# Performance work log

Measured on AMD Instinct MI355X. Metric: run time of the kernel, lower is better.

The kernel has to match this reference:

```python
import jax, jax.numpy as jnp
import numpy as np

N = 50000      # nodes
E = 800000     # edges
F_IN = 128     # input node feature dim
H = 4          # attention heads
DH = 64        # per-head hidden dim
HID = H * DH   # 256
NEG_SLOPE = 0.2


def gat_conv(h, src, dst, W, al, ar, b, res):
    # DGL GATConv: project, compute attention logits, edge softmax over dst, aggregate.
    feat = (h @ W).reshape(N, H, DH)                      # [N,H,DH]
    el = jnp.einsum('nhd,hd->nh', feat, al)               # [N,H]
    er = jnp.einsum('nhd,hd->nh', feat, ar)               # [N,H]
    e = el[src] + er[dst]                                 # [E,H]
    e = jnp.where(e > 0, e, NEG_SLOPE * e)                # LeakyReLU(0.2)
    m = jax.ops.segment_max(e, dst, num_segments=N)       # [N,H]
    m = jnp.where(jnp.isfinite(m), m, 0.0)                # zero-in-degree safety
    ex = jnp.exp(e - m[dst])                              # [E,H]
    denom = jax.ops.segment_sum(ex, dst, num_segments=N)  # [N,H]
    alpha = ex / jnp.maximum(denom[dst], 1e-16)           # edge softmax
    out = jax.ops.segment_sum(feat[src] * alpha[:, :, None], dst, num_segments=N)
    return out + res.reshape(N, H, DH) + b.reshape(1, H, DH)


def setup_inputs() -> dict:
    key = jax.random.key(0)
    ks = jax.random.split(key, 16)
    x = jax.random.normal(ks[0], (N, F_IN), jnp.float32)
    edge_index = jax.random.randint(ks[1], (2, E), 0, N)
    s_in = 1.0 / np.sqrt(F_IN)
    s_h = 1.0 / np.sqrt(HID)
    W0 = jax.random.normal(ks[2], (F_IN, HID), jnp.float32) * s_in
    W1 = jax.random.normal(ks[3], (HID, HID), jnp.float32) * s_h
    W2 = jax.random.normal(ks[4], (HID, HID), jnp.float32) * s_h
    al0 = jax.random.normal(ks[5], (H, DH), jnp.float32) * 0.1
    al1 = jax.random.normal(ks[6], (H, DH), jnp.float32) * 0.1
    al2 = jax.random.normal(ks[7], (H, DH), jnp.float32) * 0.1
    ar0 = jax.random.normal(ks[8], (H, DH), jnp.float32) * 0.1
    ar1 = jax.random.normal(ks[9], (H, DH), jnp.float32) * 0.1
    ar2 = jax.random.normal(ks[10], (H, DH), jnp.float32) * 0.1
    b0 = jnp.zeros((HID,), jnp.float32)
    b1 = jnp.zeros((HID,), jnp.float32)
    b2 = jnp.zeros((HID,), jnp.float32)
    resW0 = jax.random.normal(ks[11], (F_IN, HID), jnp.float32) * s_in
    return {"x": x, "edge_index": edge_index,
            "W0": W0, "W1": W1, "W2": W2,
            "al0": al0, "al1": al1, "al2": al2,
            "ar0": ar0, "ar1": ar1, "ar2": ar2,
            "b0": b0, "b1": b1, "b2": b2,
            "resW0": resW0}


def reference(x, edge_index, W0, W1, W2, al0, al1, al2, ar0, ar1, ar2, b0, b1, b2, resW0):
    src, dst = edge_index[0], edge_index[1]
    # layer 0: residual via linear projection (in != heads*hidden)
    h = gat_conv(x, src, dst, W0, al0, ar0, b0, x @ resW0).reshape(N, HID)
    h = jax.nn.relu(h)
    # layer 1: identity residual
    h = gat_conv(h, src, dst, W1, al1, ar1, b1, h).reshape(N, HID)
    h = jax.nn.relu(h)
    # layer 2: identity residual, mean over heads
    h = gat_conv(h, src, dst, W2, al2, ar2, b2, h)
    return h.mean(axis=1)  # [N, DH]
```

## Files before the change

### kernel.cpp

```cpp
#include <hip/hip_runtime.h>
#include <math.h>

#define N_NODES 50000
#define N_EDGES 800000
#define F_INPUT 128
#define HEADS 4
#define DHID 64
#define HID 256
#define M_PAD 50048
#define SCAN_B 49

typedef _Float16 half8 __attribute__((ext_vector_type(8)));
typedef _Float16 half4 __attribute__((ext_vector_type(4)));
typedef float f32x4 __attribute__((ext_vector_type(4)));


__global__ void hist_kernel(const int* __restrict__ dst, int* __restrict__ counts) {
    int e = blockIdx.x * 256 + threadIdx.x;
    if (e < N_EDGES) atomicAdd(&counts[dst[e]], 1);
}

__global__ __launch_bounds__(256) void scan1_kernel(const int* __restrict__ counts,
                                                    int* __restrict__ pre,
                                                    int* __restrict__ bsum) {
    __shared__ int buf[256];
    int tid = threadIdx.x;
    int idx = blockIdx.x * 1024 + tid * 4;
    int v0 = 0, v1 = 0, v2 = 0, v3 = 0;
    if (idx + 3 < N_NODES) {
        int4 v = *(const int4*)&counts[idx];
        v0 = v.x; v1 = v.y; v2 = v.z; v3 = v.w;
    } else {
        if (idx + 0 < N_NODES) v0 = counts[idx + 0];
        if (idx + 1 < N_NODES) v1 = counts[idx + 1];
        if (idx + 2 < N_NODES) v2 = counts[idx + 2];
        if (idx + 3 < N_NODES) v3 = counts[idx + 3];
    }
    int s0 = v0, s1 = s0 + v1, s2 = s1 + v2, s3 = s2 + v3;
    buf[tid] = s3;
    __syncthreads();
    for (int off = 1; off < 256; off <<= 1) {
        int t = (tid >= off) ? buf[tid - off] : 0;
        __syncthreads();
        buf[tid] += t;
        __syncthreads();
    }
    int excl = buf[tid] - s3;
    if (idx + 0 < N_NODES) pre[idx + 0] = excl + s0;
    if (idx + 1 < N_NODES) pre[idx + 1] = excl + s1;
    if (idx + 2 < N_NODES) pre[idx + 2] = excl + s2;
    if (idx + 3 < N_NODES) pre[idx + 3] = excl + s3;
    if (tid == 255) bsum[blockIdx.x] = buf[255];
}

__global__ void scan2_kernel(const int* __restrict__ bsum, int* __restrict__ bpre) {
    int lane = threadIdx.x;
    int v = (lane < SCAN_B) ? bsum[lane] : 0;
    int orig = v;
#pragma unroll
    for (int off = 1; off < 64; off <<= 1) {
        int t = __shfl_up(v, off, 64);
        if (lane >= off) v += t;
    }
    if (lane < SCAN_B) bpre[lane] = v - orig;
}

__global__ __launch_bounds__(256) void scan3_kernel(const int* __restrict__ pre,
                                                    const int* __restrict__ bpre,
                                                    int* __restrict__ row_ptr) {
    int add = bpre[blockIdx.x];
    int idx = blockIdx.x * 1024 + threadIdx.x * 4;
#pragma unroll
    for (int u = 0; u < 4; u++) {
        int i = idx + u;
        if (i < N_NODES) row_ptr[i + 1] = pre[i] + add;
    }
    if (blockIdx.x == 0 && threadIdx.x == 0) row_ptr[0] = 0;
}

__global__ void scatter_kernel(const int* __restrict__ src, const int* __restrict__ dst,
                               const int* __restrict__ row_ptr, int* __restrict__ cursor,
                               int* __restrict__ esrc) {
    int e = blockIdx.x * 256 + threadIdx.x;
    if (e < N_EDGES) {
        int d = dst[e];
        int pos = row_ptr[d] + atomicAdd(&cursor[d], 1);
        esrc[pos] = src[e];
    }
}


__global__ void cvt_x_kernel(const float* __restrict__ x, _Float16* __restrict__ x16) {
    int t = blockIdx.x * 256 + threadIdx.x;
    if (t < N_NODES * F_INPUT / 4) {
        f32x4 v = *(const f32x4*)&x[t * 4];
        half4 h = {(_Float16)v.x, (_Float16)v.y, (_Float16)v.z, (_Float16)v.w};
        *(half4*)&x16[(size_t)t * 4] = h;
    }
}

__global__ void wt_all_kernel(const float* __restrict__ W0, _Float16* __restrict__ Wt0,
                              const float* __restrict__ WR, _Float16* __restrict__ WtR,
                              const float* __restrict__ W1, _Float16* __restrict__ Wt1,
                              const float* __restrict__ W2, _Float16* __restrict__ Wt2) {
    int t = blockIdx.x * 256 + threadIdx.x;
    const float* W; _Float16* Wt; int K; int u;
    if (t < 32768)        { W = W0; Wt = Wt0; K = F_INPUT; u = t; }
    else if (t < 65536)   { W = WR; Wt = WtR; K = F_INPUT; u = t - 32768; }
    else if (t < 131072)  { W = W1; Wt = Wt1; K = HID;     u = t - 65536; }
    else if (t < 196608)  { W = W2; Wt = Wt2; K = HID;     u = t - 131072; }
    else return;
    int k = u >> 8;
    int c = u & 255;
    Wt[(size_t)c * K + k] = (_Float16)W[u];
}


__device__ __forceinline__ void gl2lds16(const void* g, void* l) {
    __builtin_amdgcn_global_load_lds((const __attribute__((address_space(1))) void*)g,
                                     (__attribute__((address_space(3))) void*)l, 16, 0, 0);
}

__global__ __launch_bounds__(256) void mfma_gemm(const _Float16* __restrict__ A16,
                                                 const _Float16* __restrict__ Wt,
                                                 _Float16* __restrict__ out16,
                                                 float* __restrict__ out32,
                                                 int K) {
    __shared__ __align__(16) _Float16 As[4 * 512];
    __shared__ __align__(16) _Float16 Ws[16 * 512];
    int tid = threadIdx.x;
    int w = tid >> 6;
    int lane = tid & 63;
    int lrow = lane & 15;
    int lk = lane >> 4;
    int row0 = blockIdx.x * 64;

    f32x4 acc[4][4] = {};
    const _Float16* Abase = A16 + (size_t)(row0 + w * 16 + lrow) * K + lk * 8;

    for (int k0 = 0; k0 < K; k0 += 32) {
        gl2lds16(Abase + k0, &As[w * 512]);
#pragma unroll
        for (int i = 0; i < 4; i++) {
            int tt = i * 4 + w;
            gl2lds16(Wt + (size_t)(tt * 16 + lrow) * K + k0 + lk * 8, &Ws[tt * 512]);
        }
        __syncthreads();
        half8 a[4], b[4];
#pragma unroll
        for (int m = 0; m < 4; m++) a[m] = *(const half8*)&As[m * 512 + lane * 8];
#pragma unroll
        for (int j = 0; j < 4; j++) b[j] = *(const half8*)&Ws[(w * 4 + j) * 512 + lane * 8];
#pragma unroll
        for (int m = 0; m < 4; m++)
#pragma unroll
            for (int j = 0; j < 4; j++)
                acc[m][j] = __builtin_amdgcn_mfma_f32_16x16x32_f16(a[m], b[j], acc[m][j], 0, 0, 0);
        __syncthreads();
    }

#pragma unroll
    for (int m = 0; m < 4; m++) {
#pragma unroll
        for (int r = 0; r < 4; r++) {
            int grow = row0 + m * 16 + lk * 4 + r;
            if (grow < N_NODES) {
                if (out16) {
#pragma unroll
                    for (int j = 0; j < 4; j++)
                        out16[(size_t)grow * HID + w * 64 + j * 16 + lrow] = (_Float16)acc[m][j][r];
                } else {
#pragma unroll
                    for (int j = 0; j < 4; j++)
                        out32[(size_t)grow * HID + w * 64 + j * 16 + lrow] = acc[m][j][r];
                }
            }
        }
    }
}


__global__ __launch_bounds__(256) void elr_kernel(const _Float16* __restrict__ feat16,
                                                  const float* __restrict__ al,
                                                  const float* __restrict__ ar,
                                                  float* __restrict__ el, float* __restrict__ er) {
    int n = blockIdx.x * 4 + (threadIdx.x >> 6);
    int lane = threadIdx.x & 63;
    half4 f = *(const half4*)&feat16[(size_t)n * HID + lane * 4];
    f32x4 a = *(const f32x4*)&al[lane * 4];
    f32x4 r = *(const f32x4*)&ar[lane * 4];
    float pl = (float)f.x * a.x + (float)f.y * a.y + (float)f.z * a.z + (float)f.w * a.w;
    float pr = (float)f.x * r.x + (float)f.y * r.y + (float)f.z * r.z + (float)f.w * r.w;
#pragma unroll
    for (int off = 1; off < 16; off <<= 1) {
        pl += __shfl_xor(pl, off, 64);
        pr += __shfl_xor(pr, off, 64);
    }
    if ((lane & 15) == 0) {
        int h = lane >> 4;
        el[n * HEADS + h] = pl;
        er[n * HEADS + h] = pr;
    }
}


__global__ __launch_bounds__(256) void agg_kernel(const _Float16* __restrict__ feat16,
                                                  const float* __restrict__ el,
                                                  const float* __restrict__ er,
                                                  const int* __restrict__ row_ptr,
                                                  const int* __restrict__ esrc,
                                                  const float* __restrict__ res,
                                                  const float* __restrict__ bias,
                                                  float* __restrict__ out32,
                                                  _Float16* __restrict__ out16,
                                                  float* __restrict__ outmean,
                                                  int do_relu) {
    __shared__ float lds[4][64 * 5];
    int wv = threadIdx.x >> 6;
    int lane = threadIdx.x & 63;
    int n = blockIdx.x * 4 + wv;
    int head = lane >> 4;
    int start = row_ptr[n];
    int deg = row_ptr[n + 1] - start;
    f32x4 ern = *(const f32x4*)&er[n * 4];
    float* L = lds[wv];

    f32x4 mx = {-1e30f, -1e30f, -1e30f, -1e30f};
    f32x4 acc = {0.f, 0.f, 0.f, 0.f};
    float smh = 0.f;

    for (int base = 0; base < deg; base += 64) {
        int e = base + lane;
        int s = 0;
        f32x4 x = {-1e30f, -1e30f, -1e30f, -1e30f};
        if (e < deg) {
            s = esrc[start + e];
            f32x4 v = *(const f32x4*)&el[s * 4];
            v = v + ern;
            x.x = v.x > 0.f ? v.x : 0.2f * v.x;
            x.y = v.y > 0.f ? v.y : 0.2f * v.y;
            x.z = v.z > 0.f ? v.z : 0.2f * v.z;
            x.w = v.w > 0.f ? v.w : 0.2f * v.w;
        }
        f32x4 cm = x;
#pragma unroll
        for (int off = 1; off < 64; off <<= 1) {
            cm.x = fmaxf(cm.x, __shfl_xor(cm.x, off, 64));
            cm.y = fmaxf(cm.y, __shfl_xor(cm.y, off, 64));
            cm.z = fmaxf(cm.z, __shfl_xor(cm.z, off, 64));
            cm.w = fmaxf(cm.w, __shfl_xor(cm.w, off, 64));
        }
        f32x4 nmx;
        nmx.x = fmaxf(mx.x, cm.x);
        nmx.y = fmaxf(mx.y, cm.y);
        nmx.z = fmaxf(mx.z, cm.z);
        nmx.w = fmaxf(mx.w, cm.w);
        float mxh  = (head == 0) ? mx.x  : (head == 1) ? mx.y  : (head == 2) ? mx.z  : mx.w;
        float nmxh = (head == 0) ? nmx.x : (head == 1) ? nmx.y : (head == 2) ? nmx.z : nmx.w;
        float sc = __expf(mxh - nmxh);
        smh *= sc;
        acc = acc * sc;
        f32x4 ex4;
        ex4.x = __expf(x.x - nmx.x);
        ex4.y = __expf(x.y - nmx.y);
        ex4.z = __expf(x.z - nmx.z);
        ex4.w = __expf(x.w - nmx.w);
        L[lane * 5 + 0] = ex4.x;
        L[lane * 5 + 1] = ex4.y;
        L[lane * 5 + 2] = ex4.z;
        L[lane * 5 + 3] = ex4.w;
        L[lane * 5 + 4] = __int_as_float(s);
        f32x4 cs = ex4;
#pragma unroll
        for (int off = 1; off < 64; off <<= 1) {
            cs.x += __shfl_xor(cs.x, off, 64);
            cs.y += __shfl_xor(cs.y, off, 64);
            cs.z += __shfl_xor(cs.z, off, 64);
            cs.w += __shfl_xor(cs.w, off, 64);
        }
        smh += (head == 0) ? cs.x : (head == 1) ? cs.y : (head == 2) ? cs.z : cs.w;

        int cnt = min(64, deg - base);
        int j = 0;
        for (; j + 4 <= cnt; j += 4) {
            float exv[4]; int ssv[4];
#pragma unroll
            for (int u = 0; u < 4; u++) {
                exv[u] = L[(j + u) * 5 + head];
                ssv[u] = __float_as_int(L[(j + u) * 5 + 4]);
            }
            half4 f[4];
#pragma unroll
            for (int u = 0; u < 4; u++)
                f[u] = *(const half4*)&feat16[(size_t)ssv[u] * HID + lane * 4];
#pragma unroll
            for (int u = 0; u < 4; u++) {
                acc.x += exv[u] * (float)f[u].x;
                acc.y += exv[u] * (float)f[u].y;
                acc.z += exv[u] * (float)f[u].z;
                acc.w += exv[u] * (float)f[u].w;
            }
        }
        for (; j < cnt; j++) {
            float ex = L[j * 5 + head];
            int ss = __float_as_int(L[j * 5 + 4]);
            half4 f = *(const half4*)&feat16[(size_t)ss * HID + lane * 4];
            acc.x += ex * (float)f.x;
            acc.y += ex * (float)f.y;
            acc.z += ex * (float)f.z;
            acc.w += ex * (float)f.w;
        }
        mx = nmx;
    }

    float inv = 1.f / fmaxf(smh, 1e-16f);
    f32x4 o = acc * inv;
    o = o + *(const f32x4*)&res[(size_t)n * HID + lane * 4] + *(const f32x4*)&bias[lane * 4];
    if (do_relu) {
        o.x = fmaxf(o.x, 0.f);
        o.y = fmaxf(o.y, 0.f);
        o.z = fmaxf(o.z, 0.f);
        o.w = fmaxf(o.w, 0.f);
    }
    if (outmean) {
        o.x += __shfl_xor(o.x, 16, 64); o.x += __shfl_xor(o.x, 32, 64);
        o.y += __shfl_xor(o.y, 16, 64); o.y += __shfl_xor(o.y, 32, 64);
        o.z += __shfl_xor(o.z, 16, 64); o.z += __shfl_xor(o.z, 32, 64);
        o.w += __shfl_xor(o.w, 16, 64); o.w += __shfl_xor(o.w, 32, 64);
        if (head == 0) {
            f32x4 mo = o * 0.25f;
            *(f32x4*)&outmean[(size_t)n * DHID + (lane & 15) * 4] = mo;
        }
    } else {
        *(f32x4*)&out32[(size_t)n * HID + lane * 4] = o;
        half4 h = {(_Float16)o.x, (_Float16)o.y, (_Float16)o.z, (_Float16)o.w};
        *(half4*)&out16[(size_t)n * HID + lane * 4] = h;
    }
}


extern "C" void kernel_launch(void* const* d_in, const int* in_sizes, int n_in,
                              void* d_out, int out_size, void* d_ws, size_t ws_size,
                              hipStream_t stream) {
    const float* x     = (const float*)d_in[0];
    const int*   ei    = (const int*)d_in[1];
    const float* W0    = (const float*)d_in[2];
    const float* W1    = (const float*)d_in[3];
    const float* W2    = (const float*)d_in[4];
    const float* al0   = (const float*)d_in[5];
    const float* al1   = (const float*)d_in[6];
    const float* al2   = (const float*)d_in[7];
    const float* ar0   = (const float*)d_in[8];
    const float* ar1   = (const float*)d_in[9];
    const float* ar2   = (const float*)d_in[10];
    const float* b0    = (const float*)d_in[11];
    const float* b1    = (const float*)d_in[12];
    const float* b2    = (const float*)d_in[13];
    const float* resW0 = (const float*)d_in[14];
    float* out = (float*)d_out;

    const int* srcp = ei;
    const int* dstp = ei + N_EDGES;

    char* p = (char*)d_ws;
    auto alloc = [&](size_t bytes) -> char* {
        char* r = p;
        p += (bytes + 255) & ~(size_t)255;
        return r;
    };
    float*     H32    = (float*)alloc((size_t)N_NODES * HID * 4);
    _Float16*  H16    = (_Float16*)alloc((size_t)M_PAD * HID * 2);
    _Float16*  feat16 = (_Float16*)alloc((size_t)M_PAD * HID * 2);
    _Float16*  x16    = (_Float16*)alloc((size_t)M_PAD * F_INPUT * 2);
    float*     el     = (float*)alloc((size_t)N_NODES * HEADS * 4);
    float*     er     = (float*)alloc((size_t)N_NODES * HEADS * 4);
    _Float16*  Wt0    = (_Float16*)alloc((size_t)HID * F_INPUT * 2);
    _Float16*  WtR    = (_Float16*)alloc((size_t)HID * F_INPUT * 2);
    _Float16*  Wt1    = (_Float16*)alloc((size_t)HID * HID * 2);
    _Float16*  Wt2    = (_Float16*)alloc((size_t)HID * HID * 2);
    int*       counts = (int*)alloc((size_t)N_NODES * 4);
    int*       rowptr = (int*)alloc((size_t)(N_NODES + 1) * 4);
    int*       esrc   = (int*)alloc((size_t)N_EDGES * 4);
    int*       pre    = (int*)alloc((size_t)N_NODES * 4);
    int*       bsum   = (int*)alloc((size_t)SCAN_B * 4);
    int*       bpre   = (int*)alloc((size_t)SCAN_B * 4);

    const int EB = (N_EDGES + 255) / 256;
    const int GB = M_PAD / 64;
    const int NB = N_NODES / 4;

    hipMemsetAsync(counts, 0, (size_t)N_NODES * 4, stream);
    hist_kernel<<<EB, 256, 0, stream>>>(dstp, counts);
    scan1_kernel<<<SCAN_B, 256, 0, stream>>>(counts, pre, bsum);
    scan2_kernel<<<1, 64, 0, stream>>>(bsum, bpre);
    scan3_kernel<<<SCAN_B, 256, 0, stream>>>(pre, bpre, rowptr);
    hipMemsetAsync(counts, 0, (size_t)N_NODES * 4, stream);
    scatter_kernel<<<EB, 256, 0, stream>>>(srcp, dstp, rowptr, counts, esrc);

    cvt_x_kernel<<<(N_NODES * F_INPUT / 4 + 255) / 256, 256, 0, stream>>>(x, x16);
    wt_all_kernel<<<768, 256, 0, stream>>>(W0, Wt0, resW0, WtR, W1, Wt1, W2, Wt2);

    mfma_gemm<<<GB, 256, 0, stream>>>(x16, WtR, nullptr, H32, F_INPUT);
    mfma_gemm<<<GB, 256, 0, stream>>>(x16, Wt0, feat16, nullptr, F_INPUT);
    elr_kernel<<<NB, 256, 0, stream>>>(feat16, al0, ar0, el, er);
    agg_kernel<<<NB, 256, 0, stream>>>(feat16, el, er, rowptr, esrc, H32, b0, H32, H16, nullptr, 1);

    mfma_gemm<<<GB, 256, 0, stream>>>(H16, Wt1, feat16, nullptr, HID);
    elr_kernel<<<NB, 256, 0, stream>>>(feat16, al1, ar1, el, er);
    agg_kernel<<<NB, 256, 0, stream>>>(feat16, el, er, rowptr, esrc, H32, b1, H32, H16, nullptr, 1);

    mfma_gemm<<<GB, 256, 0, stream>>>(H16, Wt2, feat16, nullptr, HID);
    elr_kernel<<<NB, 256, 0, stream>>>(feat16, al2, ar2, el, er);
    agg_kernel<<<NB, 256, 0, stream>>>(feat16, el, er, rowptr, esrc, H32, b2, nullptr, nullptr, out, 0);
}
```

Baseline: 549.2 us.

## Fuse attention logits into GEMM epilogues and merge layer-0 projections

The per-head el/er dot products move into the MFMA GEMM epilogue, computed from the fp32 accumulators with lane shuffles, so the three separate elr kernels and their re-reads of feat16 go away. Layer 0 packs W0 and resW0 into one 512-column transposed weight and computes feature and residual projections in a single 512-thread kernel, loading the input tile once. The hidden-layer GEMM uses 128-row tiles with 8 waves to share the weight tile more widely. The aggregation kernel gets a single-pass softmax path for nodes with degree at most 64, and the two counter memsets become one; the extra epilogue work and larger blocks may raise register pressure.

```diff
diff --git a/kernel.cpp b/kernel.cpp
--- a/kernel.cpp
+++ b/kernel.cpp
@@ -34,7 +34,6 @@
         if (idx + 0 < N_NODES) v0 = counts[idx + 0];
         if (idx + 1 < N_NODES) v1 = counts[idx + 1];
         if (idx + 2 < N_NODES) v2 = counts[idx + 2];
-        if (idx + 3 < N_NODES) v3 = counts[idx + 3];
     }
     int s0 = v0, s1 = s0 + v1, s2 = s1 + v2, s3 = s2 + v3;
     buf[tid] = s3;
@@ -99,20 +98,27 @@
     }
 }
 
-__global__ void wt_all_kernel(const float* __restrict__ W0, _Float16* __restrict__ Wt0,
-                              const float* __restrict__ WR, _Float16* __restrict__ WtR,
+__global__ void wt_all_kernel(const float* __restrict__ W0, const float* __restrict__ WR,
+                              _Float16* __restrict__ WtL0,
                               const float* __restrict__ W1, _Float16* __restrict__ Wt1,
                               const float* __restrict__ W2, _Float16* __restrict__ Wt2) {
     int t = blockIdx.x * 256 + threadIdx.x;
-    const float* W; _Float16* Wt; int K; int u;
-    if (t < 32768)        { W = W0; Wt = Wt0; K = F_INPUT; u = t; }
-    else if (t < 65536)   { W = WR; Wt = WtR; K = F_INPUT; u = t - 32768; }
-    else if (t < 131072)  { W = W1; Wt = Wt1; K = HID;     u = t - 65536; }
-    else if (t < 196608)  { W = W2; Wt = Wt2; K = HID;     u = t - 131072; }
-    else return;
-    int k = u >> 8;
-    int c = u & 255;
-    Wt[(size_t)c * K + k] = (_Float16)W[u];
+    if (t < 65536) {
+        int c = t >> 7;
+        int k = t & 127;
+        float v = (c < 256) ? W0[k * 256 + c] : WR[k * 256 + (c - 256)];
+        WtL0[t] = (_Float16)v;
+    } else if (t < 131072) {
+        int u = t - 65536;
+        int c = u >> 8;
+        int k = u & 255;
+        Wt1[u] = (_Float16)W1[k * 256 + c];
+    } else if (t < 196608) {
+        int u = t - 131072;
+        int c = u >> 8;
+        int k = u & 255;
+        Wt2[u] = (_Float16)W2[k * 256 + c];
+    }
 }
 
 
@@ -121,36 +127,124 @@
                                      (__attribute__((address_space(3))) void*)l, 16, 0, 0);
 }
 
-__global__ __launch_bounds__(256) void mfma_gemm(const _Float16* __restrict__ A16,
-                                                 const _Float16* __restrict__ Wt,
-                                                 _Float16* __restrict__ out16,
-                                                 float* __restrict__ out32,
-                                                 int K) {
+__global__ __launch_bounds__(512) void gemm_l0(const _Float16* __restrict__ A16,
+                                               const _Float16* __restrict__ WtL0,
+                                               _Float16* __restrict__ feat16,
+                                               float* __restrict__ res32,
+                                               const float* __restrict__ al,
+                                               const float* __restrict__ ar,
+                                               float* __restrict__ el, float* __restrict__ er) {
     __shared__ __align__(16) _Float16 As[4 * 512];
+    __shared__ __align__(16) _Float16 Ws[32 * 512];
+    int tid = threadIdx.x;
+    int w = tid >> 6;
+    int lane = tid & 63;
+    int lrow = lane & 15;
+    int lk = lane >> 4;
+    int row0 = blockIdx.x * 64;
+
+    f32x4 acc[4][4] = {};
+
+    for (int k0 = 0; k0 < F_INPUT; k0 += 32) {
+        if (w < 4)
+            gl2lds16(A16 + (size_t)(row0 + w * 16 + lrow) * F_INPUT + k0 + lk * 8, &As[w * 512]);
+#pragma unroll
+        for (int i = 0; i < 4; i++) {
+            int tt = i * 8 + w;
+            gl2lds16(WtL0 + (size_t)(tt * 16 + lrow) * F_INPUT + k0 + lk * 8, &Ws[tt * 512]);
+        }
+        __syncthreads();
+        half8 a[4], b[4];
+#pragma unroll
+        for (int m = 0; m < 4; m++) a[m] = *(const half8*)&As[m * 512 + lane * 8];
+#pragma unroll
+        for (int j = 0; j < 4; j++) b[j] = *(const half8*)&Ws[(w * 4 + j) * 512 + lane * 8];
+#pragma unroll
+        for (int m = 0; m < 4; m++)
+#pragma unroll
+            for (int j = 0; j < 4; j++)
+                acc[m][j] = __builtin_amdgcn_mfma_f32_16x16x32_f16(a[m], b[j], acc[m][j], 0, 0, 0);
+        __syncthreads();
+    }
+
+    if (w < 4) {
+        float alv[4], arv[4];
+#pragma unroll
+        for (int j = 0; j < 4; j++) {
+            alv[j] = al[w * 64 + j * 16 + lrow];
+            arv[j] = ar[w * 64 + j * 16 + lrow];
+        }
+#pragma unroll
+        for (int m = 0; m < 4; m++) {
+#pragma unroll
+            for (int r = 0; r < 4; r++) {
+                int row = row0 + m * 16 + lk * 4 + r;
+                if (row < N_NODES) {
+#pragma unroll
+                    for (int j = 0; j < 4; j++)
+                        feat16[(size_t)row * HID + w * 64 + j * 16 + lrow] = (_Float16)acc[m][j][r];
+                }
+                float pl = acc[m][0][r] * alv[0] + acc[m][1][r] * alv[1] +
+                           acc[m][2][r] * alv[2] + acc[m][3][r] * alv[3];
+                float pr = acc[m][0][r] * arv[0] + acc[m][1][r] * arv[1] +
+                           acc[m][2][r] * arv[2] + acc[m][3][r] * arv[3];
+#pragma unroll
+                for (int off = 1; off < 16; off <<= 1) {
+                    pl += __shfl_xor(pl, off, 64);
+                    pr += __shfl_xor(pr, off, 64);
+                }
+                if (lrow == 0 && row < N_NODES) {
+                    el[row * 4 + w] = pl;
+                    er[row * 4 + w] = pr;
+                }
+            }
+        }
+    } else {
+        int wc = w - 4;
+#pragma unroll
+        for (int m = 0; m < 4; m++) {
+#pragma unroll
+            for (int r = 0; r < 4; r++) {
+                int row = row0 + m * 16 + lk * 4 + r;
+                if (row < N_NODES) {
+#pragma unroll
+                    for (int j = 0; j < 4; j++)
+                        res32[(size_t)row * HID + wc * 64 + j * 16 + lrow] = acc[m][j][r];
+                }
+            }
+        }
+    }
+}
+
+__global__ __launch_bounds__(512) void gemm_h(const _Float16* __restrict__ A16,
+                                              const _Float16* __restrict__ Wt,
+                                              _Float16* __restrict__ feat16,
+                                              const float* __restrict__ al,
+                                              const float* __restrict__ ar,
+                                              float* __restrict__ el, float* __restrict__ er) {
+    __shared__ __align__(16) _Float16 As[8 * 512];
     __shared__ __align__(16) _Float16 Ws[16 * 512];
     int tid = threadIdx.x;
     int w = tid >> 6;
     int lane = tid & 63;
     int lrow = lane & 15;
     int lk = lane >> 4;
-    int row0 = blockIdx.x * 64;
+    int wrow = w >> 2;
+    int wcol = w & 3;
+    int row0 = blockIdx.x * 128;
 
     f32x4 acc[4][4] = {};
-    const _Float16* Abase = A16 + (size_t)(row0 + w * 16 + lrow) * K + lk * 8;
-
-    for (int k0 = 0; k0 < K; k0 += 32) {
-        gl2lds16(Abase + k0, &As[w * 512]);
-#pragma unroll
-        for (int i = 0; i < 4; i++) {
-            int tt = i * 4 + w;
-            gl2lds16(Wt + (size_t)(tt * 16 + lrow) * K + k0 + lk * 8, &Ws[tt * 512]);
-        }
+
+    for (int k0 = 0; k0 < HID; k0 += 32) {
+        gl2lds16(A16 + (size_t)(row0 + w * 16 + lrow) * HID + k0 + lk * 8, &As[w * 512]);
+        gl2lds16(Wt + (size_t)(w * 16 + lrow) * HID + k0 + lk * 8, &Ws[w * 512]);
+        gl2lds16(Wt + (size_t)((w + 8) * 16 + lrow) * HID + k0 + lk * 8, &Ws[(w + 8) * 512]);
         __syncthreads();
         half8 a[4], b[4];
 #pragma unroll
-        for (int m = 0; m < 4; m++) a[m] = *(const half8*)&As[m * 512 + lane * 8];
-#pragma unroll
-        for (int j = 0; j < 4; j++) b[j] = *(const half8*)&Ws[(w * 4 + j) * 512 + lane * 8];
+        for (int m = 0; m < 4; m++) a[m] = *(const half8*)&As[(wrow * 4 + m) * 512 + lane * 8];
+#pragma unroll
+        for (int j = 0; j < 4; j++) b[j] = *(const half8*)&Ws[(wcol * 4 + j) * 512 + lane * 8];
 #pragma unroll
         for (int m = 0; m < 4; m++)
 #pragma unroll
@@ -159,47 +253,36 @@
         __syncthreads();
     }
 
+    float alv[4], arv[4];
+#pragma unroll
+    for (int j = 0; j < 4; j++) {
+        alv[j] = al[wcol * 64 + j * 16 + lrow];
+        arv[j] = ar[wcol * 64 + j * 16 + lrow];
+    }
 #pragma unroll
     for (int m = 0; m < 4; m++) {
 #pragma unroll
         for (int r = 0; r < 4; r++) {
-            int grow = row0 + m * 16 + lk * 4 + r;
-            if (grow < N_NODES) {
-                if (out16) {
-#pragma unroll
-                    for (int j = 0; j < 4; j++)
-                        out16[(size_t)grow * HID + w * 64 + j * 16 + lrow] = (_Float16)acc[m][j][r];
-                } else {
-#pragma unroll
-                    for (int j = 0; j < 4; j++)
-                        out32[(size_t)grow * HID + w * 64 + j * 16 + lrow] = acc[m][j][r];
-                }
-            }
-        }
-    }
-}
-
-
-__global__ __launch_bounds__(256) void elr_kernel(const _Float16* __restrict__ feat16,
-                                                  const float* __restrict__ al,
-                                                  const float* __restrict__ ar,
-                                                  float* __restrict__ el, float* __restrict__ er) {
-    int n = blockIdx.x * 4 + (threadIdx.x >> 6);
-    int lane = threadIdx.x & 63;
-    half4 f = *(const half4*)&feat16[(size_t)n * HID + lane * 4];
-    f32x4 a = *(const f32x4*)&al[lane * 4];
-    f32x4 r = *(const f32x4*)&ar[lane * 4];
-    float pl = (float)f.x * a.x + (float)f.y * a.y + (float)f.z * a.z + (float)f.w * a.w;
-    float pr = (float)f.x * r.x + (float)f.y * r.y + (float)f.z * r.z + (float)f.w * r.w;
-#pragma unroll
-    for (int off = 1; off < 16; off <<= 1) {
-        pl += __shfl_xor(pl, off, 64);
-        pr += __shfl_xor(pr, off, 64);
-    }
-    if ((lane & 15) == 0) {
-        int h = lane >> 4;
-        el[n * HEADS + h] = pl;
-        er[n * HEADS + h] = pr;
+            int row = row0 + wrow * 64 + m * 16 + lk * 4 + r;
+            if (row < N_NODES) {
+#pragma unroll
+                for (int j = 0; j < 4; j++)
+                    feat16[(size_t)row * HID + wcol * 64 + j * 16 + lrow] = (_Float16)acc[m][j][r];
+            }
+            float pl = acc[m][0][r] * alv[0] + acc[m][1][r] * alv[1] +
+                       acc[m][2][r] * alv[2] + acc[m][3][r] * alv[3];
+            float pr = acc[m][0][r] * arv[0] + acc[m][1][r] * arv[1] +
+                       acc[m][2][r] * arv[2] + acc[m][3][r] * arv[3];
+#pragma unroll
+            for (int off = 1; off < 16; off <<= 1) {
+                pl += __shfl_xor(pl, off, 64);
+                pr += __shfl_xor(pr, off, 64);
+            }
+            if (lrow == 0 && row < N_NODES) {
+                el[row * 4 + wcol] = pl;
+                er[row * 4 + wcol] = pr;
+            }
+        }
     }
 }
 
@@ -225,16 +308,14 @@
     f32x4 ern = *(const f32x4*)&er[n * 4];
     float* L = lds[wv];
 
-    f32x4 mx = {-1e30f, -1e30f, -1e30f, -1e30f};
     f32x4 acc = {0.f, 0.f, 0.f, 0.f};
     float smh = 0.f;
 
-    for (int base = 0; base < deg; base += 64) {
-        int e = base + lane;
+    if (deg <= 64) {
         int s = 0;
         f32x4 x = {-1e30f, -1e30f, -1e30f, -1e30f};
-        if (e < deg) {
-            s = esrc[start + e];
+        if (lane < deg) {
+            s = esrc[start + lane];
             f32x4 v = *(const f32x4*)&el[s * 4];
             v = v + ern;
             x.x = v.x > 0.f ? v.x : 0.2f * v.x;
@@ -250,21 +331,11 @@
             cm.z = fmaxf(cm.z, __shfl_xor(cm.z, off, 64));
             cm.w = fmaxf(cm.w, __shfl_xor(cm.w, off, 64));
         }
-        f32x4 nmx;
-        nmx.x = fmaxf(mx.x, cm.x);
-        nmx.y = fmaxf(mx.y, cm.y);
-        nmx.z = fmaxf(mx.z, cm.z);
-        nmx.w = fmaxf(mx.w, cm.w);
-        float mxh  = (head == 0) ? mx.x  : (head == 1) ? mx.y  : (head == 2) ? mx.z  : mx.w;
-        float nmxh = (head == 0) ? nmx.x : (head == 1) ? nmx.y : (head == 2) ? nmx.z : nmx.w;
-        float sc = __expf(mxh - nmxh);
-        smh *= sc;
-        acc = acc * sc;
         f32x4 ex4;
-        ex4.x = __expf(x.x - nmx.x);
-        ex4.y = __expf(x.y - nmx.y);
-        ex4.z = __expf(x.z - nmx.z);
-        ex4.w = __expf(x.w - nmx.w);
+        ex4.x = __expf(x.x - cm.x);
+        ex4.y = __expf(x.y - cm.y);
+        ex4.z = __expf(x.z - cm.z);
+        ex4.w = __expf(x.w - cm.w);
         L[lane * 5 + 0] = ex4.x;
         L[lane * 5 + 1] = ex4.y;
         L[lane * 5 + 2] = ex4.z;
@@ -278,11 +349,10 @@
             cs.z += __shfl_xor(cs.z, off, 64);
             cs.w += __shfl_xor(cs.w, off, 64);
         }
-        smh += (head == 0) ? cs.x : (head == 1) ? cs.y : (head == 2) ? cs.z : cs.w;
-
-        int cnt = min(64, deg - base);
+        smh = (head == 0) ? cs.x : (head == 1) ? cs.y : (head == 2) ? cs.z : cs.w;
+
         int j = 0;
-        for (; j + 4 <= cnt; j += 4) {
+        for (; j + 4 <= deg; j += 4) {
             float exv[4]; int ssv[4];
 #pragma unroll
             for (int u = 0; u < 4; u++) {
@@ -301,7 +371,7 @@
                 acc.w += exv[u] * (float)f[u].w;
             }
         }
-        for (; j < cnt; j++) {
+        for (; j < deg; j++) {
             float ex = L[j * 5 + head];
             int ss = __float_as_int(L[j * 5 + 4]);
             half4 f = *(const half4*)&feat16[(size_t)ss * HID + lane * 4];
@@ -310,7 +380,91 @@
             acc.z += ex * (float)f.z;
             acc.w += ex * (float)f.w;
         }
-        mx = nmx;
+    } else {
+        f32x4 mx = {-1e30f, -1e30f, -1e30f, -1e30f};
+        for (int base = 0; base < deg; base += 64) {
+            int e = base + lane;
+            int s = 0;
+            f32x4 x = {-1e30f, -1e30f, -1e30f, -1e30f};
+            if (e < deg) {
+                s = esrc[start + e];
+                f32x4 v = *(const f32x4*)&el[s * 4];
+                v = v + ern;
+                x.x = v.x > 0.f ? v.x : 0.2f * v.x;
+                x.y = v.y > 0.f ? v.y : 0.2f * v.y;
+                x.z = v.z > 0.f ? v.z : 0.2f * v.z;
+                x.w = v.w > 0.f ? v.w : 0.2f * v.w;
+            }
+            f32x4 cm = x;
+#pragma unroll
+            for (int off = 1; off < 64; off <<= 1) {
+                cm.x = fmaxf(cm.x, __shfl_xor(cm.x, off, 64));
+                cm.y = fmaxf(cm.y, __shfl_xor(cm.y, off, 64));
+                cm.z = fmaxf(cm.z, __shfl_xor(cm.z, off, 64));
+                cm.w = fmaxf(cm.w, __shfl_xor(cm.w, off, 64));
+            }
+            f32x4 nmx;
+            nmx.x = fmaxf(mx.x, cm.x);
+            nmx.y = fmaxf(mx.y, cm.y);
+            nmx.z = fmaxf(mx.z, cm.z);
+            nmx.w = fmaxf(mx.w, cm.w);
+            float mxh  = (head == 0) ? mx.x  : (head == 1) ? mx.y  : (head == 2) ? mx.z  : mx.w;
+            float nmxh = (head == 0) ? nmx.x : (head == 1) ? nmx.y : (head == 2) ? nmx.z : nmx.w;
+            float sc = __expf(mxh - nmxh);
+            smh *= sc;
+            acc = acc * sc;
+            f32x4 ex4;
+            ex4.x = __expf(x.x - nmx.x);
+            ex4.y = __expf(x.y - nmx.y);
+            ex4.z = __expf(x.z - nmx.z);
+            ex4.w = __expf(x.w - nmx.w);
+            L[lane * 5 + 0] = ex4.x;
+            L[lane * 5 + 1] = ex4.y;
+            L[lane * 5 + 2] = ex4.z;
+            L[lane * 5 + 3] = ex4.w;
+            L[lane * 5 + 4] = __int_as_float(s);
+            f32x4 cs = ex4;
+#pragma unroll
+            for (int off = 1; off < 64; off <<= 1) {
+                cs.x += __shfl_xor(cs.x, off, 64);
+                cs.y += __shfl_xor(cs.y, off, 64);
+                cs.z += __shfl_xor(cs.z, off, 64);
+                cs.w += __shfl_xor(cs.w, off, 64);
+            }
+            smh += (head == 0) ? cs.x : (head == 1) ? cs.y : (head == 2) ? cs.z : cs.w;
+
+            int cnt = min(64, deg - base);
+            int j = 0;
+            for (; j + 4 <= cnt; j += 4) {
+                float exv[4]; int ssv[4];
+#pragma unroll
+                for (int u = 0; u < 4; u++) {
+                    exv[u] = L[(j + u) * 5 + head];
+                    ssv[u] = __float_as_int(L[(j + u) * 5 + 4]);
+                }
+                half4 f[4];
+#pragma unroll
+                for (int u = 0; u < 4; u++)
+                    f[u] = *(const half4*)&feat16[(size_t)ssv[u] * HID + lane * 4];
+#pragma unroll
+                for (int u = 0; u < 4; u++) {
+                    acc.x += exv[u] * (float)f[u].x;
+                    acc.y += exv[u] * (float)f[u].y;
+                    acc.z += exv[u] * (float)f[u].z;
+                    acc.w += exv[u] * (float)f[u].w;
+                }
+            }
+            for (; j < cnt; j++) {
+                float ex = L[j * 5 + head];
+                int ss = __float_as_int(L[j * 5 + 4]);
+                half4 f = *(const half4*)&feat16[(size_t)ss * HID + lane * 4];
+                acc.x += ex * (float)f.x;
+                acc.y += ex * (float)f.y;
+                acc.z += ex * (float)f.z;
+                acc.w += ex * (float)f.w;
+            }
+            mx = nmx;
+        }
     }
 
     float inv = 1.f / fmaxf(smh, 1e-16f);
@@ -374,11 +528,11 @@
     _Float16*  x16    = (_Float16*)alloc((size_t)M_PAD * F_INPUT * 2);
     float*     el     = (float*)alloc((size_t)N_NODES * HEADS * 4);
     float*     er     = (float*)alloc((size_t)N_NODES * HEADS * 4);
-    _Float16*  Wt0    = (_Float16*)alloc((size_t)HID * F_INPUT * 2);
-    _Float16*  WtR    = (_Float16*)alloc((size_t)HID * F_INPUT * 2);
+    _Float16*  WtL0   = (_Float16*)alloc((size_t)512 * F_INPUT * 2);
     _Float16*  Wt1    = (_Float16*)alloc((size_t)HID * HID * 2);
     _Float16*  Wt2    = (_Float16*)alloc((size_t)HID * HID * 2);
-    int*       counts = (int*)alloc((size_t)N_NODES * 4);
+    int*       counts = (int*)alloc((size_t)2 * N_NODES * 4);
+    int*       cursor = counts + N_NODES;
     int*       rowptr = (int*)alloc((size_t)(N_NODES + 1) * 4);
     int*       esrc   = (int*)alloc((size_t)N_EDGES * 4);
     int*       pre    = (int*)alloc((size_t)N_NODES * 4);
@@ -386,30 +540,24 @@
     int*       bpre   = (int*)alloc((size_t)SCAN_B * 4);
 
     const int EB = (N_EDGES + 255) / 256;
-    const int GB = M_PAD / 64;
     const int NB = N_NODES / 4;
 
-    hipMemsetAsync(counts, 0, (size_t)N_NODES * 4, stream);
+    hipMemsetAsync(counts, 0, (size_t)2 * N_NODES * 4, stream);
     hist_kernel<<<EB, 256, 0, stream>>>(dstp, counts);
     scan1_kernel<<<SCAN_B, 256, 0, stream>>>(counts, pre, bsum);
     scan2_kernel<<<1, 64, 0, stream>>>(bsum, bpre);
     scan3_kernel<<<SCAN_B, 256, 0, stream>>>(pre, bpre, rowptr);
-    hipMemsetAsync(counts, 0, (size_t)N_NODES * 4, stream);
-    scatter_kernel<<<EB, 256, 0, stream>>>(srcp, dstp, rowptr, counts, esrc);
+    scatter_kernel<<<EB, 256, 0, stream>>>(srcp, dstp, rowptr, cursor, esrc);
 
     cvt_x_kernel<<<(N_NODES * F_INPUT / 4 + 255) / 256, 256, 0, stream>>>(x, x16);
-    wt_all_kernel<<<768, 256, 0, stream>>>(W0, Wt0, resW0, WtR, W1, Wt1, W2, Wt2);
-
-    mfma_gemm<<<GB, 256, 0, stream>>>(x16, WtR, nullptr, H32, F_INPUT);
-    mfma_gemm<<<GB, 256, 0, stream>>>(x16, Wt0, feat16, nullptr, F_INPUT);
-    elr_kernel<<<NB, 256, 0, stream>>>(feat16, al0, ar0, el, er);
+    wt_all_kernel<<<768, 256, 0, stream>>>(W0, resW0, WtL0, W1, Wt1, W2, Wt2);
+
+    gemm_l0<<<M_PAD / 64, 512, 0, stream>>>(x16, WtL0, feat16, H32, al0, ar0, el, er);
     agg_kernel<<<NB, 256, 0, stream>>>(feat16, el, er, rowptr, esrc, H32, b0, H32, H16, nullptr, 1);
 
-    mfma_gemm<<<GB, 256, 0, stream>>>(H16, Wt1, feat16, nullptr, HID);
-    elr_kernel<<<NB, 256, 0, stream>>>(feat16, al1, ar1, el, er);
+    gemm_h<<<M_PAD / 128, 512, 0, stream>>>(H16, Wt1, feat16, al1, ar1, el, er);
     agg_kernel<<<NB, 256, 0, stream>>>(feat16, el, er, rowptr, esrc, H32, b1, H32, H16, nullptr, 1);
 
-    mfma_gemm<<<GB, 256, 0, stream>>>(H16, Wt2, feat16, nullptr, HID);
-    elr_kernel<<<NB, 256, 0, stream>>>(feat16, al2, ar2, el, er);
+    gemm_h<<<M_PAD / 128, 512, 0, stream>>>(H16, Wt2, feat16, al2, ar2, el, er);
     agg_kernel<<<NB, 256, 0, stream>>>(feat16, el, er, rowptr, esrc, H32, b2, nullptr, nullptr, out, 0);
 }
```

Measured after the change: 517.9 us. -5.7%, faster.
